# Kernel optimization log

Hardware: AMD Instinct MI355X
Metric: run time of the kernel (lower is better)

The kernel has to match this reference:

```python
import jax, jax.numpy as jnp
import numpy as np

V = 100000      # num nodes
E = 600000      # num edges (even: first half in-edges, second half out-edges)
D_IN = 128
D_OUT = 128
NREL2 = 100     # num_rel * 2
BN_EPS = 1e-5


def ccorr(a, b):
    # circular correlation along last dim: irfft(conj(rfft(a)) * rfft(b), n=d)
    d = a.shape[-1]
    return jnp.fft.irfft(jnp.conj(jnp.fft.rfft(a)) * jnp.fft.rfft(b), n=d).astype(a.dtype)


def setup_inputs() -> dict:
    key = jax.random.key(0)
    ks = jax.random.split(key, 12)
    return {
        "x": jax.random.normal(ks[0], (V, D_IN), dtype=jnp.float32),
        "rel_repr": jax.random.normal(ks[1], (NREL2, D_IN), dtype=jnp.float32),
        "edge_norm": jax.random.uniform(ks[2], (E,), dtype=jnp.float32),
        "in_w": jax.random.normal(ks[3], (D_IN, D_OUT), dtype=jnp.float32) * 0.05,
        "out_w": jax.random.normal(ks[4], (D_IN, D_OUT), dtype=jnp.float32) * 0.05,
        "loop_w": jax.random.normal(ks[5], (D_IN, D_OUT), dtype=jnp.float32) * 0.05,
        "w_rel": jax.random.normal(ks[6], (D_IN, D_OUT), dtype=jnp.float32) * 0.05,
        "loop_rel": jax.random.normal(ks[7], (1, D_IN), dtype=jnp.float32),
        "bias": jnp.zeros((D_OUT,), dtype=jnp.float32),
        "bn_gamma": jnp.ones((D_OUT,), dtype=jnp.float32),
        "bn_beta": jnp.zeros((D_OUT,), dtype=jnp.float32),
        "edge_src": jax.random.randint(ks[8], (E,), 0, V, dtype=jnp.int32),
        "edge_dst": jax.random.randint(ks[9], (E,), 0, V, dtype=jnp.int32),
        "edge_type": jax.random.randint(ks[10], (E,), 0, NREL2, dtype=jnp.int32),
    }


def reference(x, rel_repr, edge_norm, in_w, out_w, loop_w, w_rel, loop_rel,
              bias, bn_gamma, bn_beta, edge_src, edge_dst, edge_type):
    rel = rel_repr  # rel_wt is None (num_base=-1)
    # gather src features per edge and compose with relation embedding (corr)
    edge_data = ccorr(x[edge_src], rel[edge_type])             # [E, D_IN]
    half = edge_data.shape[0] // 2
    msg = jnp.concatenate(
        [edge_data[:half] @ in_w, edge_data[half:] @ out_w], axis=0
    ) * edge_norm[:, None]                                     # [E, D_OUT]
    # scatter-sum into destination nodes
    agg = jax.ops.segment_sum(msg, edge_dst, num_segments=V)   # [V, D_OUT]
    # self-loop term
    loop = ccorr(x, jnp.broadcast_to(loop_rel, x.shape)) @ loop_w
    h = (agg + loop) / 3.0 + bias
    # BatchNorm1d (training mode: batch stats, biased variance)
    mean = h.mean(axis=0)
    var = h.var(axis=0)
    h = (h - mean) * jax.lax.rsqrt(var + BN_EPS) * bn_gamma + bn_beta
    # act is identity; ltr=True -> project relations
    return h, rel @ w_rel
```

## Files before the change

kernel.cpp:

```cpp
#include <hip/hip_runtime.h>
#include <hip/hip_bf16.h>

#define D 128
constexpr int V_N    = 100000;
constexpr int E_N    = 600000;
constexpr int HALF_E = E_N / 2;
constexpr int NREL2  = 100;
constexpr int NBUCK  = 2 * NREL2;
constexpr float BN_EPS_F = 1e-5f;

constexpr int CHUNK  = 4096;
constexpr int NCHUNK = (E_N + CHUNK - 1) / CHUNK;

typedef short bf16x8  __attribute__((ext_vector_type(8)));
typedef float f32x16  __attribute__((ext_vector_type(16)));
typedef float f32x4v  __attribute__((ext_vector_type(4)));
typedef unsigned int uint32;

constexpr size_t MT_BYTES  = 201ull * D * D * 2;
constexpr size_t P_SS_OFF  = MT_BYTES;
constexpr size_t P_SD_OFF  = P_SS_OFF + (size_t)E_N * 4;
constexpr size_t P_SN_OFF  = P_SD_OFF + (size_t)E_N * 4;
constexpr size_t P_AGG_OFF = P_SN_OFF + (size_t)E_N * 4;
constexpr size_t AGG_BYTES = (size_t)V_N * D * 2;
constexpr size_t P_HIST_OFF = P_AGG_OFF;
constexpr size_t P_COFF_OFF = P_HIST_OFF + (size_t)NBUCK * NCHUNK * 4;
constexpr size_t P_CS_OFF  = P_AGG_OFF + AGG_BYTES;
constexpr size_t P_CQ_OFF  = P_CS_OFF + 512;
constexpr size_t P_CNT_OFF = P_CQ_OFF + 512;
constexpr size_t P_ST_OFF  = P_CNT_OFF + 1024;
constexpr size_t WS_NEED_PK = P_ST_OFF + 1024;

constexpr int LOOP_GRID2 = 782;
constexpr size_t P2_XBF  = (WS_NEED_PK + 255) & ~(size_t)255;
constexpr size_t P2_PSUM = P2_XBF + AGG_BYTES;
constexpr size_t P2_PSQ  = P2_PSUM + 128ull * LOOP_GRID2 * 4;
constexpr size_t WS_NEED2 = P2_PSQ + 128ull * LOOP_GRID2 * 4;

__device__ inline unsigned short f2bf(float f) {
    __hip_bfloat16 h = __float2bfloat16(f);
    return __builtin_bit_cast(unsigned short, h);
}
__device__ inline float bf2f(unsigned int u) {
    return __uint_as_float(u << 16);
}

__device__ inline int bucket_of(int e, const int* __restrict__ etype) {
    return etype[e] + (e < HALF_E ? 0 : NREL2);
}

__global__ __launch_bounds__(256) void k_hist_chunk(const int* __restrict__ etype,
                                                    int* __restrict__ hist) {
    __shared__ int h[NBUCK];
    for (int i = threadIdx.x; i < NBUCK; i += 256) h[i] = 0;
    __syncthreads();
    int c = blockIdx.x;
    int e0 = c * CHUNK;
#pragma unroll
    for (int r = 0; r < CHUNK / 256; r++) {
        int e = e0 + r * 256 + threadIdx.x;
        if (e < E_N) atomicAdd(&h[bucket_of(e, etype)], 1);
    }
    __syncthreads();
    for (int b = threadIdx.x; b < NBUCK; b += 256) hist[b * NCHUNK + c] = h[b];
}

__global__ void k_scan_bucket(const int* __restrict__ hist, int* __restrict__ chunkoff,
                              int* __restrict__ counts) {
    int b = blockIdx.x, lane = threadIdx.x;
    int acc = 0;
    for (int base = 0; base < NCHUNK; base += 64) {
        int c = base + lane;
        int v = (c < NCHUNK) ? hist[b * NCHUNK + c] : 0;
        int s = v;
#pragma unroll
        for (int off = 1; off < 64; off <<= 1) {
            int t = __shfl(s, lane - off, 64);
            if (lane >= off) s += t;
        }
        if (c < NCHUNK) chunkoff[b * NCHUNK + c] = acc + (s - v);
        acc += __shfl(s, 63, 64);
    }
    if (lane == 0) counts[b] = acc;
}

__global__ void k_scan(const int* __restrict__ counts, int* __restrict__ starts) {
    __shared__ int s[256];
    int i = threadIdx.x;
    int v = (i < NBUCK) ? counts[i] : 0;
    s[i] = v;
    __syncthreads();
    for (int off = 1; off < 256; off <<= 1) {
        int t = (i >= off) ? s[i - off] : 0;
        __syncthreads();
        s[i] += t;
        __syncthreads();
    }
    if (i < NBUCK) starts[i] = s[i] - v;
    if (i == 255) starts[NBUCK] = s[255];
}

__global__ __launch_bounds__(256) void k_scatter2(
    const int* __restrict__ src, const int* __restrict__ dst,
    const float* __restrict__ norm, const int* __restrict__ etype,
    const int* __restrict__ starts, const int* __restrict__ chunkoff,
    int* __restrict__ ssrc, int* __restrict__ sdst, float* __restrict__ snorm) {
    __shared__ int h[NBUCK];
    __shared__ int sbase[NBUCK];
    int c = blockIdx.x;
    for (int b = threadIdx.x; b < NBUCK; b += 256) {
        h[b] = 0;
        sbase[b] = starts[b] + chunkoff[b * NCHUNK + c];
    }
    __syncthreads();
    int e0 = c * CHUNK;
#pragma unroll
    for (int r = 0; r < CHUNK / 256; r++) {
        int e = e0 + r * 256 + threadIdx.x;
        if (e < E_N) {
            int b = bucket_of(e, etype);
            int rank = atomicAdd(&h[b], 1);
            int p = sbase[b] + rank;
            ssrc[p] = src[e]; sdst[p] = dst[e]; snorm[p] = norm[e];
        }
    }
}

__global__ __launch_bounds__(256) void k_xbf(const float* __restrict__ x,
                                             ushort* __restrict__ xbf) {
    const int N8 = V_N * D / 8;
    int i = blockIdx.x * 256 + threadIdx.x;
    if (i >= N8) return;
    f32x4v v0 = *(const f32x4v*)&x[(size_t)i * 8];
    f32x4v v1 = *(const f32x4v*)&x[(size_t)i * 8 + 4];
    union { ushort u[8]; uint4 q; } t;
    t.u[0] = f2bf(v0[0]); t.u[1] = f2bf(v0[1]); t.u[2] = f2bf(v0[2]); t.u[3] = f2bf(v0[3]);
    t.u[4] = f2bf(v1[0]); t.u[5] = f2bf(v1[1]); t.u[6] = f2bf(v1[2]); t.u[7] = f2bf(v1[3]);
    *(uint4*)&xbf[(size_t)i * 8] = t.q;
}

__global__ void k_build_M(const float* __restrict__ rel, const float* __restrict__ in_w,
                          const float* __restrict__ out_w, const float* __restrict__ loop_rel,
                          const float* __restrict__ loop_w, ushort* __restrict__ MT) {
    extern __shared__ float smem[];
    float* sW = smem;
    float* sR = smem + D * D;
    int b = blockIdx.x;
    const float* r = (b < NREL2) ? rel + (size_t)b * D
                   : (b < NBUCK) ? rel + (size_t)(b - NREL2) * D : loop_rel;
    const float* W = (b < NREL2) ? in_w : (b < NBUCK) ? out_w : loop_w;
    for (int i = threadIdx.x; i < D * D; i += blockDim.x) sW[i] = W[i];
    for (int i = threadIdx.x; i < D; i += blockDim.x) { float v = r[i]; sR[i] = v; sR[i + D] = v; }
    __syncthreads();
    int o  = threadIdx.x & 127;
    int jg = threadIdx.x >> 7;
    ushort* MTb = MT + (size_t)b * (D * D);
    for (int pass = 0; pass < 4; pass++) {
        int jbase = jg * 64 + pass * 16;
        float acc[16];
#pragma unroll
        for (int t = 0; t < 16; t++) acc[t] = 0.f;
        for (int k = 0; k < D; k++) {
            float w = sW[k * D + o];
#pragma unroll
            for (int t = 0; t < 16; t++) acc[t] += sR[jbase + t + k] * w;
        }
#pragma unroll
        for (int t = 0; t < 16; t++) MTb[(size_t)o * D + jbase + t] = f2bf(acc[t]);
    }
}

__global__ void k_relw(const float* __restrict__ rel, const float* __restrict__ w_rel,
                       float* __restrict__ out2) {
    int rr = blockIdx.x, o = threadIdx.x;
    float acc = 0.f;
    for (int k = 0; k < D; k++) acc += rel[rr * D + k] * w_rel[k * D + o];
    out2[rr * D + o] = acc;
}

constexpr int BPB = 8;

__global__ __launch_bounds__(256) void k_edge_pkb(
    const ushort* __restrict__ xbf, const ushort* __restrict__ MT,
    const int* __restrict__ starts, const int* __restrict__ ssrc,
    const int* __restrict__ sdst, const float* __restrict__ snorm,
    ushort* __restrict__ agg) {
    int wid  = threadIdx.x >> 6, lane = threadIdx.x & 63;
    int l31  = lane & 31, l5 = lane >> 5;
    int bucket = blockIdx.x / BPB;
    int sib    = (blockIdx.x % BPB) * 2 + (wid >> 1);
    int oh     = wid & 1;
    int bstart = starts[bucket], bend = starts[bucket + 1];
    const ushort* MTb = MT + (size_t)bucket * (D * D);
    int c0 = oh * 64 + 2 * l31;
    bf16x8 B0[8], B1[8];
#pragma unroll
    for (int kc = 0; kc < 8; kc++) {
        B0[kc] = *(const bf16x8*)&MTb[(size_t)c0 * D + kc * 16 + l5 * 8];
        B1[kc] = *(const bf16x8*)&MTb[(size_t)(c0 + 1) * D + kc * 16 + l5 * 8];
    }
    for (int tbase = bstart + sib * 32; tbase < bend; tbase += BPB * 2 * 32) {
        int nv = bend - tbase; if (nv > 32) nv = 32;
        int sr = ssrc[tbase + (l31 < nv ? l31 : 0)];
        const ushort* xr = xbf + (size_t)sr * D + l5 * 8;
        bf16x8 A[8];
#pragma unroll
        for (int kc = 0; kc < 8; kc++) A[kc] = *(const bf16x8*)(xr + kc * 16);
        f32x16 C0, C1;
#pragma unroll
        for (int i = 0; i < 16; i++) { C0[i] = 0.f; C1[i] = 0.f; }
#pragma unroll
        for (int kc = 0; kc < 8; kc++) {
            C0 = __builtin_amdgcn_mfma_f32_32x32x16_bf16(A[kc], B0[kc], C0, 0, 0, 0);
            C1 = __builtin_amdgcn_mfma_f32_32x32x16_bf16(A[kc], B1[kc], C1, 0, 0, 0);
        }
#pragma unroll
        for (int r = 0; r < 16; r++) {
            int rw = (r & 3) + 8 * (r >> 2) + 4 * l5;
            if (rw < nv) {
                float nm = snorm[tbase + rw];
                int   dv = sdst[tbase + rw];
                union { ushort u[2]; unsigned int w; } p;
                p.u[0] = f2bf(C0[r] * nm);
                p.u[1] = f2bf(C1[r] * nm);
                ushort* ap = agg + (size_t)dv * D + c0;
                asm volatile("global_atomic_pk_add_bf16 %0, %1, off"
                             :: "v"(ap), "v"(p.w) : "memory");
            }
        }
    }
}

__global__ __launch_bounds__(256) void k_loop_nb(
    const ushort* __restrict__ xbf, const ushort* __restrict__ MT,
    const float* __restrict__ bias, const ushort* __restrict__ agg,
    float* __restrict__ out, float* __restrict__ psum, float* __restrict__ psq) {
    __shared__ float lsum[128], lsq[128];
    if (threadIdx.x < 128) { lsum[threadIdx.x] = 0.f; lsq[threadIdx.x] = 0.f; }
    int wid = threadIdx.x >> 6, lane = threadIdx.x & 63;
    int l31 = lane & 31, l5 = lane >> 5;
    int oh  = wid & 1;
    int strm = blockIdx.x * 2 + (wid >> 1);
    const int NSTR = LOOP_GRID2 * 2;
    const ushort* MTb = MT + (size_t)NBUCK * (D * D);
    int ocol0 = oh * 64 + l31, ocol1 = oh * 64 + 32 + l31;
    bf16x8 B0[8], B1[8];
#pragma unroll
    for (int kc = 0; kc < 8; kc++) {
        B0[kc] = *(const bf16x8*)&MTb[(size_t)ocol0 * D + kc * 16 + l5 * 8];
        B1[kc] = *(const bf16x8*)&MTb[(size_t)ocol1 * D + kc * 16 + l5 * 8];
    }
    float b0 = bias[ocol0], b1 = bias[ocol1];
    float ps0 = 0.f, pq0 = 0.f, ps1 = 0.f, pq1 = 0.f;
    const int NT = V_N / 32;
    for (int tile = strm; tile < NT; tile += NSTR) {
        int tbase = tile * 32;
        const ushort* xr = xbf + (size_t)(tbase + l31) * D + l5 * 8;
        bf16x8 A[8];
#pragma unroll
        for (int kc = 0; kc < 8; kc++) A[kc] = *(const bf16x8*)(xr + kc * 16);
        f32x16 C0, C1;
#pragma unroll
        for (int i = 0; i < 16; i++) { C0[i] = 0.f; C1[i] = 0.f; }
#pragma unroll
        for (int kc = 0; kc < 8; kc++) {
            C0 = __builtin_amdgcn_mfma_f32_32x32x16_bf16(A[kc], B0[kc], C0, 0, 0, 0);
            C1 = __builtin_amdgcn_mfma_f32_32x32x16_bf16(A[kc], B1[kc], C1, 0, 0, 0);
        }
#pragma unroll
        for (int r = 0; r < 16; r++) {
            int rw = (r & 3) + 8 * (r >> 2) + 4 * l5;
            size_t i0 = (size_t)(tbase + rw) * D + ocol0;
            size_t i1 = (size_t)(tbase + rw) * D + ocol1;
            float h0 = (bf2f((uint32)agg[i0]) + C0[r]) * (1.f / 3.f) + b0;
            float h1 = (bf2f((uint32)agg[i1]) + C1[r]) * (1.f / 3.f) + b1;
            out[i0] = h0; out[i1] = h1;
            ps0 += h0; pq0 += h0 * h0;
            ps1 += h1; pq1 += h1 * h1;
        }
    }
    __syncthreads();
    atomicAdd(&lsum[ocol0], ps0); atomicAdd(&lsq[ocol0], pq0);
    atomicAdd(&lsum[ocol1], ps1); atomicAdd(&lsq[ocol1], pq1);
    __syncthreads();
    if (threadIdx.x < 128) {
        psum[(size_t)threadIdx.x * LOOP_GRID2 + blockIdx.x] = lsum[threadIdx.x];
        psq [(size_t)threadIdx.x * LOOP_GRID2 + blockIdx.x] = lsq [threadIdx.x];
    }
}

__global__ __launch_bounds__(256) void k_colreduce(
    const float* __restrict__ psum, const float* __restrict__ psq,
    float* __restrict__ colsum, float* __restrict__ colsq) {
    __shared__ float ls[256], lq[256];
    int c = blockIdx.x, tid = threadIdx.x;
    float s = 0.f, q = 0.f;
    for (int b = tid; b < LOOP_GRID2; b += 256) {
        s += psum[(size_t)c * LOOP_GRID2 + b];
        q += psq [(size_t)c * LOOP_GRID2 + b];
    }
    ls[tid] = s; lq[tid] = q;
    __syncthreads();
    for (int off = 128; off > 0; off >>= 1) {
        if (tid < off) { ls[tid] += ls[tid + off]; lq[tid] += lq[tid + off]; }
        __syncthreads();
    }
    if (tid == 0) { colsum[c] = ls[0]; colsq[c] = lq[0]; }
}

__global__ __launch_bounds__(256) void k_edge_pk(
    const float* __restrict__ x, const ushort* __restrict__ MT,
    const int* __restrict__ starts, const int* __restrict__ ssrc,
    const int* __restrict__ sdst, const float* __restrict__ snorm,
    ushort* __restrict__ agg) {
    int wid  = threadIdx.x >> 6, lane = threadIdx.x & 63;
    int l31  = lane & 31, l5 = lane >> 5;
    int bucket = blockIdx.x / BPB;
    int sib    = (blockIdx.x % BPB) * 2 + (wid >> 1);
    int oh     = wid & 1;
    int bstart = starts[bucket], bend = starts[bucket + 1];
    const ushort* MTb = MT + (size_t)bucket * (D * D);
    int c0 = oh * 64 + 2 * l31;
    bf16x8 B0[8], B1[8];
#pragma unroll
    for (int kc = 0; kc < 8; kc++) {
        B0[kc] = *(const bf16x8*)&MTb[(size_t)c0 * D + kc * 16 + l5 * 8];
        B1[kc] = *(const bf16x8*)&MTb[(size_t)(c0 + 1) * D + kc * 16 + l5 * 8];
    }
    for (int tbase = bstart + sib * 32; tbase < bend; tbase += BPB * 2 * 32) {
        int nv = bend - tbase; if (nv > 32) nv = 32;
        int sr = ssrc[tbase + (l31 < nv ? l31 : 0)];
        const float* xr = x + (size_t)sr * D + l5 * 8;
        bf16x8 A[8];
#pragma unroll
        for (int kc = 0; kc < 8; kc++) {
            f32x4v v0 = *(const f32x4v*)(xr + kc * 16);
            f32x4v v1 = *(const f32x4v*)(xr + kc * 16 + 4);
            union { bf16x8 v; ushort u[8]; } t;
            t.u[0] = f2bf(v0[0]); t.u[1] = f2bf(v0[1]); t.u[2] = f2bf(v0[2]); t.u[3] = f2bf(v0[3]);
            t.u[4] = f2bf(v1[0]); t.u[5] = f2bf(v1[1]); t.u[6] = f2bf(v1[2]); t.u[7] = f2bf(v1[3]);
            A[kc] = t.v;
        }
        f32x16 C0, C1;
#pragma unroll
        for (int i = 0; i < 16; i++) { C0[i] = 0.f; C1[i] = 0.f; }
#pragma unroll
        for (int kc = 0; kc < 8; kc++) {
            C0 = __builtin_amdgcn_mfma_f32_32x32x16_bf16(A[kc], B0[kc], C0, 0, 0, 0);
            C1 = __builtin_amdgcn_mfma_f32_32x32x16_bf16(A[kc], B1[kc], C1, 0, 0, 0);
        }
#pragma unroll
        for (int r = 0; r < 16; r++) {
            int rw = (r & 3) + 8 * (r >> 2) + 4 * l5;
            if (rw < nv) {
                float nm = snorm[tbase + rw];
                int   dv = sdst[tbase + rw];
                union { ushort u[2]; unsigned int w; } p;
                p.u[0] = f2bf(C0[r] * nm);
                p.u[1] = f2bf(C1[r] * nm);
                ushort* ap = agg + (size_t)dv * D + c0;
                asm volatile("global_atomic_pk_add_bf16 %0, %1, off"
                             :: "v"(ap), "v"(p.w) : "memory");
            }
        }
    }
}

constexpr int LOOP_GRID = 400;
__global__ __launch_bounds__(256) void k_loop_pk(
    const float* __restrict__ x, const ushort* __restrict__ MT,
    const float* __restrict__ bias, const ushort* __restrict__ agg,
    float* __restrict__ out, float* __restrict__ colsum, float* __restrict__ colsq) {
    int wid = threadIdx.x >> 6, lane = threadIdx.x & 63;
    int l31 = lane & 31, l5 = lane >> 5;
    int oh  = wid & 1;
    int strm = blockIdx.x * 2 + (wid >> 1);
    const int NSTR = LOOP_GRID * 2;
    const ushort* MTb = MT + (size_t)NBUCK * (D * D);
    int ocol0 = oh * 64 + l31, ocol1 = oh * 64 + 32 + l31;
    bf16x8 B0[8], B1[8];
#pragma unroll
    for (int kc = 0; kc < 8; kc++) {
        B0[kc] = *(const bf16x8*)&MTb[(size_t)ocol0 * D + kc * 16 + l5 * 8];
        B1[kc] = *(const bf16x8*)&MTb[(size_t)ocol1 * D + kc * 16 + l5 * 8];
    }
    float b0 = bias[ocol0], b1 = bias[ocol1];
    float ps0 = 0.f, pq0 = 0.f, ps1 = 0.f, pq1 = 0.f;
    const int NT = V_N / 32;
    for (int tile = strm; tile < NT; tile += NSTR) {
        int tbase = tile * 32;
        const float* xr = x + (size_t)(tbase + l31) * D + l5 * 8;
        bf16x8 A[8];
#pragma unroll
        for (int kc = 0; kc < 8; kc++) {
            f32x4v v0 = *(const f32x4v*)(xr + kc * 16);
            f32x4v v1 = *(const f32x4v*)(xr + kc * 16 + 4);
            union { bf16x8 v; ushort u[8]; } t;
            t.u[0] = f2bf(v0[0]); t.u[1] = f2bf(v0[1]); t.u[2] = f2bf(v0[2]); t.u[3] = f2bf(v0[3]);
            t.u[4] = f2bf(v1[0]); t.u[5] = f2bf(v1[1]); t.u[6] = f2bf(v1[2]); t.u[7] = f2bf(v1[3]);
            A[kc] = t.v;
        }
        f32x16 C0, C1;
#pragma unroll
        for (int i = 0; i < 16; i++) { C0[i] = 0.f; C1[i] = 0.f; }
#pragma unroll
        for (int kc = 0; kc < 8; kc++) {
            C0 = __builtin_amdgcn_mfma_f32_32x32x16_bf16(A[kc], B0[kc], C0, 0, 0, 0);
            C1 = __builtin_amdgcn_mfma_f32_32x32x16_bf16(A[kc], B1[kc], C1, 0, 0, 0);
        }
#pragma unroll
        for (int r = 0; r < 16; r++) {
            int rw = (r & 3) + 8 * (r >> 2) + 4 * l5;
            size_t i0 = (size_t)(tbase + rw) * D + ocol0;
            size_t i1 = (size_t)(tbase + rw) * D + ocol1;
            float h0 = (bf2f((uint32)agg[i0]) + C0[r]) * (1.f / 3.f) + b0;
            float h1 = (bf2f((uint32)agg[i1]) + C1[r]) * (1.f / 3.f) + b1;
            out[i0] = h0; out[i1] = h1;
            ps0 += h0; pq0 += h0 * h0;
            ps1 += h1; pq1 += h1 * h1;
        }
    }
    atomicAdd(&colsum[ocol0], ps0); atomicAdd(&colsq[ocol0], pq0);
    atomicAdd(&colsum[ocol1], ps1); atomicAdd(&colsq[ocol1], pq1);
}

__global__ void k_bn(float* __restrict__ out, const float* __restrict__ colsum,
                     const float* __restrict__ colsq, const float* __restrict__ gamma,
                     const float* __restrict__ beta) {
    const size_t N4 = (size_t)V_N * D / 4;
    size_t stride = (size_t)gridDim.x * blockDim.x;
    for (size_t q = (size_t)blockIdx.x * blockDim.x + threadIdx.x; q < N4; q += stride) {
        int c4 = (int)(q & 31);
        float4 s  = *(const float4*)&colsum[c4 * 4];
        float4 sq = *(const float4*)&colsq[c4 * 4];
        float4 g  = *(const float4*)&gamma[c4 * 4];
        float4 be = *(const float4*)&beta[c4 * 4];
        float4 h  = *(float4*)&out[q * 4];
        const float inv = 1.f / (float)V_N;
        float m0 = s.x * inv, m1 = s.y * inv, m2 = s.z * inv, m3 = s.w * inv;
        float r0 = rsqrtf(sq.x * inv - m0 * m0 + BN_EPS_F);
        float r1 = rsqrtf(sq.y * inv - m1 * m1 + BN_EPS_F);
        float r2 = rsqrtf(sq.z * inv - m2 * m2 + BN_EPS_F);
        float r3 = rsqrtf(sq.w * inv - m3 * m3 + BN_EPS_F);
        h.x = (h.x - m0) * r0 * g.x + be.x;
        h.y = (h.y - m1) * r1 * g.y + be.y;
        h.z = (h.z - m2) * r2 * g.z + be.z;
        h.w = (h.w - m3) * r3 * g.w + be.w;
        *(float4*)&out[q * 4] = h;
    }
}

extern "C" void kernel_launch(void* const* d_in, const int* in_sizes, int n_in,
                              void* d_out, int out_size, void* d_ws, size_t ws_size,
                              hipStream_t stream) {
    const float* x        = (const float*)d_in[0];
    const float* rel      = (const float*)d_in[1];
    const float* enorm    = (const float*)d_in[2];
    const float* in_w     = (const float*)d_in[3];
    const float* out_w    = (const float*)d_in[4];
    const float* loop_w   = (const float*)d_in[5];
    const float* w_rel    = (const float*)d_in[6];
    const float* loop_rel = (const float*)d_in[7];
    const float* bias     = (const float*)d_in[8];
    const float* gamma    = (const float*)d_in[9];
    const float* beta     = (const float*)d_in[10];
    const int*   esrc     = (const int*)d_in[11];
    const int*   edst     = (const int*)d_in[12];
    const int*   etype    = (const int*)d_in[13];
    float* out = (float*)d_out;
    char*  ws  = (char*)d_ws;

    const int gM = 201, smem = (D * D + 256) * sizeof(float);

    ushort* MT     = (ushort*)(ws + 0);
    int*    ssrc   = (int*)(ws + P_SS_OFF);
    int*    sdst   = (int*)(ws + P_SD_OFF);
    float*  snorm  = (float*)(ws + P_SN_OFF);
    ushort* aggbf  = (ushort*)(ws + P_AGG_OFF);
    int*    hist   = (int*)(ws + P_HIST_OFF);
    int*    coff   = (int*)(ws + P_COFF_OFF);
    float*  colsum = (float*)(ws + P_CS_OFF);
    float*  colsq  = (float*)(ws + P_CQ_OFF);
    int*    counts = (int*)(ws + P_CNT_OFF);
    int*    starts = (int*)(ws + P_ST_OFF);

    k_hist_chunk<<<NCHUNK, 256, 0, stream>>>(etype, hist);
    k_scan_bucket<<<NBUCK, 64, 0, stream>>>(hist, coff, counts);
    k_scan<<<1, 256, 0, stream>>>(counts, starts);
    k_scatter2<<<NCHUNK, 256, 0, stream>>>(esrc, edst, enorm, etype, starts, coff,
                                           ssrc, sdst, snorm);
    hipMemsetAsync(ws + P_AGG_OFF, 0, AGG_BYTES, stream);

    k_build_M<<<gM, 256, smem, stream>>>(rel, in_w, out_w, loop_rel, loop_w, MT);
    k_relw<<<NREL2, D, 0, stream>>>(rel, w_rel, out + (size_t)V_N * D);

    if (ws_size >= WS_NEED2) {
        ushort* xbf  = (ushort*)(ws + P2_XBF);
        float*  psum = (float*)(ws + P2_PSUM);
        float*  psq  = (float*)(ws + P2_PSQ);

        k_xbf<<<(V_N * D / 8 + 255) / 256, 256, 0, stream>>>(x, xbf);
        k_edge_pkb<<<NBUCK * BPB, 256, 0, stream>>>(xbf, MT, starts, ssrc, sdst, snorm, aggbf);
        k_loop_nb<<<LOOP_GRID2, 256, 0, stream>>>(xbf, MT, bias, aggbf, out, psum, psq);
        k_colreduce<<<128, 256, 0, stream>>>(psum, psq, colsum, colsq);
        k_bn<<<2048, 256, 0, stream>>>(out, colsum, colsq, gamma, beta);
    } else {
        hipMemsetAsync(ws + P_CS_OFF, 0, 1024, stream);
        k_edge_pk<<<NBUCK * BPB, 256, 0, stream>>>(x, MT, starts, ssrc, sdst, snorm, aggbf);
        k_loop_pk<<<LOOP_GRID, 256, 0, stream>>>(x, MT, bias, aggbf, out, colsum, colsq);
        k_bn<<<2048, 256, 0, stream>>>(out, colsum, colsq, gamma, beta);
    }
}
```

Baseline: 458.6 us.

## Replace bf16 atomic scatter with CSR segmented sum over stored messages

Adds a path, used when the workspace is large enough, that builds a CSR (degree count, scan, permutation) over destination nodes. The edge GEMM then writes per-edge bf16 messages to a buffer, and a per-node kernel sums them in fp32 with no atomics. It also merges the M-matrix build, the relation projection and the x-to-bf16 conversion into one setup launch. The loop kernel now uses a paired-column layout so agg reads and out writes are vectorised. The cost is a 150MB message buffer written then read back, several extra CSR-build kernels, and random gathers in the segmented sum. The path is skipped if the workspace is too small.

Measured after the change: 507.2 us. 10.6% more time.

```diff
diff --git a/kernel.cpp b/kernel.cpp
--- a/kernel.cpp
+++ b/kernel.cpp
@@ -17,12 +17,14 @@
 typedef float f32x4v  __attribute__((ext_vector_type(4)));
 typedef unsigned int uint32;
 
+constexpr int LOOP_GRID2 = 782;
 constexpr size_t MT_BYTES  = 201ull * D * D * 2;
+constexpr size_t AGG_BYTES = (size_t)V_N * D * 2;
+
 constexpr size_t P_SS_OFF  = MT_BYTES;
 constexpr size_t P_SD_OFF  = P_SS_OFF + (size_t)E_N * 4;
 constexpr size_t P_SN_OFF  = P_SD_OFF + (size_t)E_N * 4;
 constexpr size_t P_AGG_OFF = P_SN_OFF + (size_t)E_N * 4;
-constexpr size_t AGG_BYTES = (size_t)V_N * D * 2;
 constexpr size_t P_HIST_OFF = P_AGG_OFF;
 constexpr size_t P_COFF_OFF = P_HIST_OFF + (size_t)NBUCK * NCHUNK * 4;
 constexpr size_t P_CS_OFF  = P_AGG_OFF + AGG_BYTES;
@@ -30,13 +32,35 @@
 constexpr size_t P_CNT_OFF = P_CQ_OFF + 512;
 constexpr size_t P_ST_OFF  = P_CNT_OFF + 1024;
 constexpr size_t WS_NEED_PK = P_ST_OFF + 1024;
-
-constexpr int LOOP_GRID2 = 782;
 constexpr size_t P2_XBF  = (WS_NEED_PK + 255) & ~(size_t)255;
 constexpr size_t P2_PSUM = P2_XBF + AGG_BYTES;
 constexpr size_t P2_PSQ  = P2_PSUM + 128ull * LOOP_GRID2 * 4;
 constexpr size_t WS_NEED2 = P2_PSQ + 128ull * LOOP_GRID2 * 4;
 
+constexpr size_t V4_SS   = MT_BYTES;
+constexpr size_t V4_SD   = V4_SS + (size_t)E_N * 4;
+constexpr size_t V4_SN   = V4_SD + (size_t)E_N * 4;
+constexpr size_t V4_XBF  = V4_SN + (size_t)E_N * 4;
+constexpr size_t V4_AGG  = V4_XBF + AGG_BYTES;
+constexpr size_t V4_DEG  = V4_AGG + AGG_BYTES;
+constexpr size_t V4_CS   = V4_DEG + (size_t)V_N * 4;
+constexpr size_t V4_CQ   = V4_CS + 512;
+constexpr size_t V4_RP   = V4_CQ + 512;
+constexpr size_t V4_CUR  = V4_RP + (size_t)(V_N + 16) * 4;
+constexpr size_t V4_EIDX = V4_CUR + (size_t)V_N * 4;
+constexpr size_t V4_HIST = V4_EIDX + (size_t)E_N * 4;
+constexpr size_t V4_COFF = V4_HIST + (size_t)NBUCK * NCHUNK * 4;
+constexpr size_t V4_CNT  = V4_COFF + (size_t)NBUCK * NCHUNK * 4;
+constexpr size_t V4_ST   = V4_CNT + 1024;
+constexpr size_t V4_BSUM = V4_ST + 1024;
+constexpr size_t V4_PSUM = (V4_BSUM + 1024 + 255) & ~(size_t)255;
+constexpr size_t V4_PSQ  = V4_PSUM + 128ull * LOOP_GRID2 * 4;
+constexpr size_t V4_MSG  = (V4_PSQ + 128ull * LOOP_GRID2 * 4 + 255) & ~(size_t)255;
+constexpr size_t WS_NEED4 = V4_MSG + (size_t)E_N * D * 2;
+
+constexpr int SCAN_ELEMS = 1024;
+constexpr int NSCANB = (V_N + SCAN_ELEMS - 1) / SCAN_ELEMS;
+
 __device__ inline unsigned short f2bf(float f) {
     __hip_bfloat16 h = __float2bfloat16(f);
     return __builtin_bit_cast(unsigned short, h);
@@ -44,7 +68,6 @@
 __device__ inline float bf2f(unsigned int u) {
     return __uint_as_float(u << 16);
 }
-
 __device__ inline int bucket_of(int e, const int* __restrict__ etype) {
     return etype[e] + (e < HALF_E ? 0 : NREL2);
 }
@@ -126,59 +149,267 @@
     }
 }
 
-__global__ __launch_bounds__(256) void k_xbf(const float* __restrict__ x,
-                                             ushort* __restrict__ xbf) {
-    const int N8 = V_N * D / 8;
+constexpr int SETUP_XBF_BLOCKS = 800;
+constexpr int SETUP_GRID = 201 + 50 + SETUP_XBF_BLOCKS;
+__global__ void k_setup(const float* __restrict__ x, const float* __restrict__ rel,
+                        const float* __restrict__ in_w, const float* __restrict__ out_w,
+                        const float* __restrict__ loop_rel, const float* __restrict__ loop_w,
+                        const float* __restrict__ w_rel, ushort* __restrict__ MT,
+                        ushort* __restrict__ xbf, float* __restrict__ out2) {
+    extern __shared__ float smem[];
+    int blk = blockIdx.x;
+    if (blk < 201) {
+        float* sW = smem;
+        float* sR = smem + D * D;
+        int b = blk;
+        const float* r = (b < NREL2) ? rel + (size_t)b * D
+                       : (b < NBUCK) ? rel + (size_t)(b - NREL2) * D : loop_rel;
+        const float* W = (b < NREL2) ? in_w : (b < NBUCK) ? out_w : loop_w;
+        for (int i = threadIdx.x; i < D * D; i += blockDim.x) sW[i] = W[i];
+        for (int i = threadIdx.x; i < D; i += blockDim.x) { float v = r[i]; sR[i] = v; sR[i + D] = v; }
+        __syncthreads();
+        int o  = threadIdx.x & 127;
+        int jg = threadIdx.x >> 7;
+        ushort* MTb = MT + (size_t)b * (D * D);
+        for (int pass = 0; pass < 4; pass++) {
+            int jbase = jg * 64 + pass * 16;
+            float acc[16];
+#pragma unroll
+            for (int t = 0; t < 16; t++) acc[t] = 0.f;
+            for (int k = 0; k < D; k++) {
+                float w = sW[k * D + o];
+#pragma unroll
+                for (int t = 0; t < 16; t++) acc[t] += sR[jbase + t + k] * w;
+            }
+#pragma unroll
+            for (int t = 0; t < 16; t++) MTb[(size_t)o * D + jbase + t] = f2bf(acc[t]);
+        }
+    } else if (blk < 251) {
+        int rr = (blk - 201) * 2 + (threadIdx.x >> 7);
+        int o  = threadIdx.x & 127;
+        float acc = 0.f;
+        for (int k = 0; k < D; k++) acc += rel[rr * D + k] * w_rel[k * D + o];
+        out2[rr * D + o] = acc;
+    } else {
+        const int N8 = V_N * D / 8;
+        for (int i = (blk - 251) * 256 + threadIdx.x; i < N8; i += SETUP_XBF_BLOCKS * 256) {
+            f32x4v v0 = *(const f32x4v*)&x[(size_t)i * 8];
+            f32x4v v1 = *(const f32x4v*)&x[(size_t)i * 8 + 4];
+            union { ushort u[8]; uint4 q; } t;
+            t.u[0] = f2bf(v0[0]); t.u[1] = f2bf(v0[1]); t.u[2] = f2bf(v0[2]); t.u[3] = f2bf(v0[3]);
+            t.u[4] = f2bf(v1[0]); t.u[5] = f2bf(v1[1]); t.u[6] = f2bf(v1[2]); t.u[7] = f2bf(v1[3]);
+            *(uint4*)&xbf[(size_t)i * 8] = t.q;
+        }
+    }
+}
+
+__global__ __launch_bounds__(256) void k_deg(const int* __restrict__ sdst,
+                                             int* __restrict__ deg) {
+    int p = blockIdx.x * 256 + threadIdx.x;
+    if (p < E_N) atomicAdd(&deg[sdst[p]], 1);
+}
+
+__global__ __launch_bounds__(256) void k_scan1(const int* __restrict__ deg,
+                                               int* __restrict__ rowptr,
+                                               int* __restrict__ blocksum) {
+    __shared__ int s[256];
+    int blk = blockIdx.x, tid = threadIdx.x;
+    int base = blk * SCAN_ELEMS + tid * 4;
+    int v[4]; int tot = 0;
+#pragma unroll
+    for (int j = 0; j < 4; j++) { int i = base + j; v[j] = (i < V_N) ? deg[i] : 0; tot += v[j]; }
+    s[tid] = tot;
+    __syncthreads();
+    for (int off = 1; off < 256; off <<= 1) {
+        int t = (tid >= off) ? s[tid - off] : 0;
+        __syncthreads();
+        s[tid] += t;
+        __syncthreads();
+    }
+    int run = s[tid] - tot;
+#pragma unroll
+    for (int j = 0; j < 4; j++) { int i = base + j; if (i < V_N) rowptr[i] = run; run += v[j]; }
+    if (tid == 255) blocksum[blk] = s[255];
+}
+
+__global__ void k_scan2(int* __restrict__ blocksum) {
+    __shared__ int s[128];
+    int i = threadIdx.x;
+    int v = (i < NSCANB) ? blocksum[i] : 0;
+    s[i] = v;
+    __syncthreads();
+    for (int off = 1; off < 128; off <<= 1) {
+        int t = (i >= off) ? s[i - off] : 0;
+        __syncthreads();
+        s[i] += t;
+        __syncthreads();
+    }
+    if (i < NSCANB) blocksum[i] = s[i] - v;
+}
+
+__global__ __launch_bounds__(256) void k_scan3(int* __restrict__ rowptr,
+                                               const int* __restrict__ blocksum,
+                                               int* __restrict__ cursor) {
     int i = blockIdx.x * 256 + threadIdx.x;
-    if (i >= N8) return;
-    f32x4v v0 = *(const f32x4v*)&x[(size_t)i * 8];
-    f32x4v v1 = *(const f32x4v*)&x[(size_t)i * 8 + 4];
-    union { ushort u[8]; uint4 q; } t;
-    t.u[0] = f2bf(v0[0]); t.u[1] = f2bf(v0[1]); t.u[2] = f2bf(v0[2]); t.u[3] = f2bf(v0[3]);
-    t.u[4] = f2bf(v1[0]); t.u[5] = f2bf(v1[1]); t.u[6] = f2bf(v1[2]); t.u[7] = f2bf(v1[3]);
-    *(uint4*)&xbf[(size_t)i * 8] = t.q;
-}
-
-__global__ void k_build_M(const float* __restrict__ rel, const float* __restrict__ in_w,
-                          const float* __restrict__ out_w, const float* __restrict__ loop_rel,
-                          const float* __restrict__ loop_w, ushort* __restrict__ MT) {
-    extern __shared__ float smem[];
-    float* sW = smem;
-    float* sR = smem + D * D;
-    int b = blockIdx.x;
-    const float* r = (b < NREL2) ? rel + (size_t)b * D
-                   : (b < NBUCK) ? rel + (size_t)(b - NREL2) * D : loop_rel;
-    const float* W = (b < NREL2) ? in_w : (b < NBUCK) ? out_w : loop_w;
-    for (int i = threadIdx.x; i < D * D; i += blockDim.x) sW[i] = W[i];
-    for (int i = threadIdx.x; i < D; i += blockDim.x) { float v = r[i]; sR[i] = v; sR[i + D] = v; }
-    __syncthreads();
-    int o  = threadIdx.x & 127;
-    int jg = threadIdx.x >> 7;
-    ushort* MTb = MT + (size_t)b * (D * D);
-    for (int pass = 0; pass < 4; pass++) {
-        int jbase = jg * 64 + pass * 16;
-        float acc[16];
-#pragma unroll
-        for (int t = 0; t < 16; t++) acc[t] = 0.f;
-        for (int k = 0; k < D; k++) {
-            float w = sW[k * D + o];
-#pragma unroll
-            for (int t = 0; t < 16; t++) acc[t] += sR[jbase + t + k] * w;
-        }
-#pragma unroll
-        for (int t = 0; t < 16; t++) MTb[(size_t)o * D + jbase + t] = f2bf(acc[t]);
-    }
-}
-
-__global__ void k_relw(const float* __restrict__ rel, const float* __restrict__ w_rel,
-                       float* __restrict__ out2) {
-    int rr = blockIdx.x, o = threadIdx.x;
-    float acc = 0.f;
-    for (int k = 0; k < D; k++) acc += rel[rr * D + k] * w_rel[k * D + o];
-    out2[rr * D + o] = acc;
+    if (i < V_N) {
+        int r = rowptr[i] + blocksum[i >> 10];
+        rowptr[i] = r; cursor[i] = r;
+    }
+    if (i == 0) rowptr[V_N] = E_N;
+}
+
+__global__ __launch_bounds__(256) void k_perm(const int* __restrict__ sdst,
+                                              int* __restrict__ cursor,
+                                              int* __restrict__ eidx) {
+    int p = blockIdx.x * 256 + threadIdx.x;
+    if (p < E_N) {
+        int slot = atomicAdd(&cursor[sdst[p]], 1);
+        eidx[slot] = p;
+    }
 }
 
 constexpr int BPB = 8;
+
+__global__ __launch_bounds__(256) void k_edge_st(
+    const ushort* __restrict__ xbf, const ushort* __restrict__ MT,
+    const int* __restrict__ starts, const int* __restrict__ ssrc,
+    const float* __restrict__ snorm, uint32* __restrict__ msg32) {
+    int wid  = threadIdx.x >> 6, lane = threadIdx.x & 63;
+    int l31  = lane & 31, l5 = lane >> 5;
+    int bucket = blockIdx.x / BPB;
+    int sib    = (blockIdx.x % BPB) * 2 + (wid >> 1);
+    int oh     = wid & 1;
+    int bstart = starts[bucket], bend = starts[bucket + 1];
+    const ushort* MTb = MT + (size_t)bucket * (D * D);
+    int c0 = oh * 64 + 2 * l31;
+    bf16x8 B0[8], B1[8];
+#pragma unroll
+    for (int kc = 0; kc < 8; kc++) {
+        B0[kc] = *(const bf16x8*)&MTb[(size_t)c0 * D + kc * 16 + l5 * 8];
+        B1[kc] = *(const bf16x8*)&MTb[(size_t)(c0 + 1) * D + kc * 16 + l5 * 8];
+    }
+    for (int tbase = bstart + sib * 32; tbase < bend; tbase += BPB * 2 * 32) {
+        int nv = bend - tbase; if (nv > 32) nv = 32;
+        int sr = ssrc[tbase + (l31 < nv ? l31 : 0)];
+        const ushort* xr = xbf + (size_t)sr * D + l5 * 8;
+        bf16x8 A[8];
+#pragma unroll
+        for (int kc = 0; kc < 8; kc++) A[kc] = *(const bf16x8*)(xr + kc * 16);
+        f32x16 C0, C1;
+#pragma unroll
+        for (int i = 0; i < 16; i++) { C0[i] = 0.f; C1[i] = 0.f; }
+#pragma unroll
+        for (int kc = 0; kc < 8; kc++) {
+            C0 = __builtin_amdgcn_mfma_f32_32x32x16_bf16(A[kc], B0[kc], C0, 0, 0, 0);
+            C1 = __builtin_amdgcn_mfma_f32_32x32x16_bf16(A[kc], B1[kc], C1, 0, 0, 0);
+        }
+#pragma unroll
+        for (int r = 0; r < 16; r++) {
+            int rw = (r & 3) + 8 * (r >> 2) + 4 * l5;
+            if (rw < nv) {
+                int p = tbase + rw;
+                float nm = snorm[p];
+                uint32 u = (uint32)f2bf(C0[r] * nm) | ((uint32)f2bf(C1[r] * nm) << 16);
+                msg32[(size_t)p * 64 + oh * 32 + l31] = u;
+            }
+        }
+    }
+}
+
+__global__ __launch_bounds__(256) void k_segsum(
+    const uint32* __restrict__ msg32, const int* __restrict__ eidx,
+    const int* __restrict__ rowptr, uint32* __restrict__ agg32) {
+    int v = blockIdx.x * 4 + (threadIdx.x >> 6);
+    if (v >= V_N) return;
+    int lane = threadIdx.x & 63;
+    int s = rowptr[v], e = rowptr[v + 1];
+    float a0 = 0.f, a1 = 0.f;
+    for (int i = s; i < e; i++) {
+        int p = eidx[i];
+        uint32 u = msg32[(size_t)p * 64 + lane];
+        a0 += bf2f(u & 0xffffu); a1 += bf2f(u >> 16);
+    }
+    agg32[(size_t)v * 64 + lane] = (uint32)f2bf(a0) | ((uint32)f2bf(a1) << 16);
+}
+
+__global__ __launch_bounds__(256) void k_loop_pair(
+    const ushort* __restrict__ xbf, const ushort* __restrict__ MT,
+    const float* __restrict__ bias, const uint32* __restrict__ agg32,
+    float* __restrict__ out, float* __restrict__ psum, float* __restrict__ psq) {
+    __shared__ float lsum[128], lsq[128];
+    if (threadIdx.x < 128) { lsum[threadIdx.x] = 0.f; lsq[threadIdx.x] = 0.f; }
+    int wid = threadIdx.x >> 6, lane = threadIdx.x & 63;
+    int l31 = lane & 31, l5 = lane >> 5;
+    int oh  = wid & 1;
+    int strm = blockIdx.x * 2 + (wid >> 1);
+    const int NSTR = LOOP_GRID2 * 2;
+    const ushort* MTb = MT + (size_t)NBUCK * (D * D);
+    int c0 = oh * 64 + 2 * l31;
+    int jj = oh * 32 + l31;
+    bf16x8 B0[8], B1[8];
+#pragma unroll
+    for (int kc = 0; kc < 8; kc++) {
+        B0[kc] = *(const bf16x8*)&MTb[(size_t)c0 * D + kc * 16 + l5 * 8];
+        B1[kc] = *(const bf16x8*)&MTb[(size_t)(c0 + 1) * D + kc * 16 + l5 * 8];
+    }
+    float b0 = bias[c0], b1 = bias[c0 + 1];
+    float ps0 = 0.f, pq0 = 0.f, ps1 = 0.f, pq1 = 0.f;
+    const int NT = V_N / 32;
+    for (int tile = strm; tile < NT; tile += NSTR) {
+        int tbase = tile * 32;
+        const ushort* xr = xbf + (size_t)(tbase + l31) * D + l5 * 8;
+        bf16x8 A[8];
+#pragma unroll
+        for (int kc = 0; kc < 8; kc++) A[kc] = *(const bf16x8*)(xr + kc * 16);
+        f32x16 C0, C1;
+#pragma unroll
+        for (int i = 0; i < 16; i++) { C0[i] = 0.f; C1[i] = 0.f; }
+#pragma unroll
+        for (int kc = 0; kc < 8; kc++) {
+            C0 = __builtin_amdgcn_mfma_f32_32x32x16_bf16(A[kc], B0[kc], C0, 0, 0, 0);
+            C1 = __builtin_amdgcn_mfma_f32_32x32x16_bf16(A[kc], B1[kc], C1, 0, 0, 0);
+        }
+#pragma unroll
+        for (int r = 0; r < 16; r++) {
+            int rw = (r & 3) + 8 * (r >> 2) + 4 * l5;
+            int row = tbase + rw;
+            uint32 u = agg32[(size_t)row * 64 + jj];
+            float h0 = (bf2f(u & 0xffffu) + C0[r]) * (1.f / 3.f) + b0;
+            float h1 = (bf2f(u >> 16)     + C1[r]) * (1.f / 3.f) + b1;
+            float2 hv = make_float2(h0, h1);
+            *(float2*)&out[(size_t)row * D + c0] = hv;
+            ps0 += h0; pq0 += h0 * h0;
+            ps1 += h1; pq1 += h1 * h1;
+        }
+    }
+    __syncthreads();
+    atomicAdd(&lsum[c0], ps0); atomicAdd(&lsq[c0], pq0);
+    atomicAdd(&lsum[c0 + 1], ps1); atomicAdd(&lsq[c0 + 1], pq1);
+    __syncthreads();
+    if (threadIdx.x < 128) {
+        psum[(size_t)threadIdx.x * LOOP_GRID2 + blockIdx.x] = lsum[threadIdx.x];
+        psq [(size_t)threadIdx.x * LOOP_GRID2 + blockIdx.x] = lsq [threadIdx.x];
+    }
+}
+
+__global__ __launch_bounds__(256) void k_colreduce(
+    const float* __restrict__ psum, const float* __restrict__ psq,
+    float* __restrict__ colsum, float* __restrict__ colsq) {
+    __shared__ float ls[256], lq[256];
+    int c = blockIdx.x, tid = threadIdx.x;
+    float s = 0.f, q = 0.f;
+    for (int b = tid; b < LOOP_GRID2; b += 256) {
+        s += psum[(size_t)c * LOOP_GRID2 + b];
+        q += psq [(size_t)c * LOOP_GRID2 + b];
+    }
+    ls[tid] = s; lq[tid] = q;
+    __syncthreads();
+    for (int off = 128; off > 0; off >>= 1) {
+        if (tid < off) { ls[tid] += ls[tid + off]; lq[tid] += lq[tid + off]; }
+        __syncthreads();
+    }
+    if (tid == 0) { colsum[c] = ls[0]; colsq[c] = lq[0]; }
+}
 
 __global__ __launch_bounds__(256) void k_edge_pkb(
     const ushort* __restrict__ xbf, const ushort* __restrict__ MT,
@@ -229,199 +460,6 @@
             }
         }
     }
-}
-
-__global__ __launch_bounds__(256) void k_loop_nb(
-    const ushort* __restrict__ xbf, const ushort* __restrict__ MT,
-    const float* __restrict__ bias, const ushort* __restrict__ agg,
-    float* __restrict__ out, float* __restrict__ psum, float* __restrict__ psq) {
-    __shared__ float lsum[128], lsq[128];
-    if (threadIdx.x < 128) { lsum[threadIdx.x] = 0.f; lsq[threadIdx.x] = 0.f; }
-    int wid = threadIdx.x >> 6, lane = threadIdx.x & 63;
-    int l31 = lane & 31, l5 = lane >> 5;
-    int oh  = wid & 1;
-    int strm = blockIdx.x * 2 + (wid >> 1);
-    const int NSTR = LOOP_GRID2 * 2;
-    const ushort* MTb = MT + (size_t)NBUCK * (D * D);
-    int ocol0 = oh * 64 + l31, ocol1 = oh * 64 + 32 + l31;
-    bf16x8 B0[8], B1[8];
-#pragma unroll
-    for (int kc = 0; kc < 8; kc++) {
-        B0[kc] = *(const bf16x8*)&MTb[(size_t)ocol0 * D + kc * 16 + l5 * 8];
-        B1[kc] = *(const bf16x8*)&MTb[(size_t)ocol1 * D + kc * 16 + l5 * 8];
-    }
-    float b0 = bias[ocol0], b1 = bias[ocol1];
-    float ps0 = 0.f, pq0 = 0.f, ps1 = 0.f, pq1 = 0.f;
-    const int NT = V_N / 32;
-    for (int tile = strm; tile < NT; tile += NSTR) {
-        int tbase = tile * 32;
-        const ushort* xr = xbf + (size_t)(tbase + l31) * D + l5 * 8;
-        bf16x8 A[8];
-#pragma unroll
-        for (int kc = 0; kc < 8; kc++) A[kc] = *(const bf16x8*)(xr + kc * 16);
-        f32x16 C0, C1;
-#pragma unroll
-        for (int i = 0; i < 16; i++) { C0[i] = 0.f; C1[i] = 0.f; }
-#pragma unroll
-        for (int kc = 0; kc < 8; kc++) {
-            C0 = __builtin_amdgcn_mfma_f32_32x32x16_bf16(A[kc], B0[kc], C0, 0, 0, 0);
-            C1 = __builtin_amdgcn_mfma_f32_32x32x16_bf16(A[kc], B1[kc], C1, 0, 0, 0);
-        }
-#pragma unroll
-        for (int r = 0; r < 16; r++) {
-            int rw = (r & 3) + 8 * (r >> 2) + 4 * l5;
-            size_t i0 = (size_t)(tbase + rw) * D + ocol0;
-            size_t i1 = (size_t)(tbase + rw) * D + ocol1;
-            float h0 = (bf2f((uint32)agg[i0]) + C0[r]) * (1.f / 3.f) + b0;
-            float h1 = (bf2f((uint32)agg[i1]) + C1[r]) * (1.f / 3.f) + b1;
-            out[i0] = h0; out[i1] = h1;
-            ps0 += h0; pq0 += h0 * h0;
-            ps1 += h1; pq1 += h1 * h1;
-        }
-    }
-    __syncthreads();
-    atomicAdd(&lsum[ocol0], ps0); atomicAdd(&lsq[ocol0], pq0);
-    atomicAdd(&lsum[ocol1], ps1); atomicAdd(&lsq[ocol1], pq1);
-    __syncthreads();
-    if (threadIdx.x < 128) {
-        psum[(size_t)threadIdx.x * LOOP_GRID2 + blockIdx.x] = lsum[threadIdx.x];
-        psq [(size_t)threadIdx.x * LOOP_GRID2 + blockIdx.x] = lsq [threadIdx.x];
-    }
-}
-
-__global__ __launch_bounds__(256) void k_colreduce(
-    const float* __restrict__ psum, const float* __restrict__ psq,
-    float* __restrict__ colsum, float* __restrict__ colsq) {
-    __shared__ float ls[256], lq[256];
-    int c = blockIdx.x, tid = threadIdx.x;
-    float s = 0.f, q = 0.f;
-    for (int b = tid; b < LOOP_GRID2; b += 256) {
-        s += psum[(size_t)c * LOOP_GRID2 + b];
-        q += psq [(size_t)c * LOOP_GRID2 + b];
-    }
-    ls[tid] = s; lq[tid] = q;
-    __syncthreads();
-    for (int off = 128; off > 0; off >>= 1) {
-        if (tid < off) { ls[tid] += ls[tid + off]; lq[tid] += lq[tid + off]; }
-        __syncthreads();
-    }
-    if (tid == 0) { colsum[c] = ls[0]; colsq[c] = lq[0]; }
-}
-
-__global__ __launch_bounds__(256) void k_edge_pk(
-    const float* __restrict__ x, const ushort* __restrict__ MT,
-    const int* __restrict__ starts, const int* __restrict__ ssrc,
-    const int* __restrict__ sdst, const float* __restrict__ snorm,
-    ushort* __restrict__ agg) {
-    int wid  = threadIdx.x >> 6, lane = threadIdx.x & 63;
-    int l31  = lane & 31, l5 = lane >> 5;
-    int bucket = blockIdx.x / BPB;
-    int sib    = (blockIdx.x % BPB) * 2 + (wid >> 1);
-    int oh     = wid & 1;
-    int bstart = starts[bucket], bend = starts[bucket + 1];
-    const ushort* MTb = MT + (size_t)bucket * (D * D);
-    int c0 = oh * 64 + 2 * l31;
-    bf16x8 B0[8], B1[8];
-#pragma unroll
-    for (int kc = 0; kc < 8; kc++) {
-        B0[kc] = *(const bf16x8*)&MTb[(size_t)c0 * D + kc * 16 + l5 * 8];
-        B1[kc] = *(const bf16x8*)&MTb[(size_t)(c0 + 1) * D + kc * 16 + l5 * 8];
-    }
-    for (int tbase = bstart + sib * 32; tbase < bend; tbase += BPB * 2 * 32) {
-        int nv = bend - tbase; if (nv > 32) nv = 32;
-        int sr = ssrc[tbase + (l31 < nv ? l31 : 0)];
-        const float* xr = x + (size_t)sr * D + l5 * 8;
-        bf16x8 A[8];
-#pragma unroll
-        for (int kc = 0; kc < 8; kc++) {
-            f32x4v v0 = *(const f32x4v*)(xr + kc * 16);
-            f32x4v v1 = *(const f32x4v*)(xr + kc * 16 + 4);
-            union { bf16x8 v; ushort u[8]; } t;
-            t.u[0] = f2bf(v0[0]); t.u[1] = f2bf(v0[1]); t.u[2] = f2bf(v0[2]); t.u[3] = f2bf(v0[3]);
-            t.u[4] = f2bf(v1[0]); t.u[5] = f2bf(v1[1]); t.u[6] = f2bf(v1[2]); t.u[7] = f2bf(v1[3]);
-            A[kc] = t.v;
-        }
-        f32x16 C0, C1;
-#pragma unroll
-        for (int i = 0; i < 16; i++) { C0[i] = 0.f; C1[i] = 0.f; }
-#pragma unroll
-        for (int kc = 0; kc < 8; kc++) {
-            C0 = __builtin_amdgcn_mfma_f32_32x32x16_bf16(A[kc], B0[kc], C0, 0, 0, 0);
-            C1 = __builtin_amdgcn_mfma_f32_32x32x16_bf16(A[kc], B1[kc], C1, 0, 0, 0);
-        }
-#pragma unroll
-        for (int r = 0; r < 16; r++) {
-            int rw = (r & 3) + 8 * (r >> 2) + 4 * l5;
-            if (rw < nv) {
-                float nm = snorm[tbase + rw];
-                int   dv = sdst[tbase + rw];
-                union { ushort u[2]; unsigned int w; } p;
-                p.u[0] = f2bf(C0[r] * nm);
-                p.u[1] = f2bf(C1[r] * nm);
-                ushort* ap = agg + (size_t)dv * D + c0;
-                asm volatile("global_atomic_pk_add_bf16 %0, %1, off"
-                             :: "v"(ap), "v"(p.w) : "memory");
-            }
-        }
-    }
-}
-
-constexpr int LOOP_GRID = 400;
-__global__ __launch_bounds__(256) void k_loop_pk(
-    const float* __restrict__ x, const ushort* __restrict__ MT,
-    const float* __restrict__ bias, const ushort* __restrict__ agg,
-    float* __restrict__ out, float* __restrict__ colsum, float* __restrict__ colsq) {
-    int wid = threadIdx.x >> 6, lane = threadIdx.x & 63;
-    int l31 = lane & 31, l5 = lane >> 5;
-    int oh  = wid & 1;
-    int strm = blockIdx.x * 2 + (wid >> 1);
-    const int NSTR = LOOP_GRID * 2;
-    const ushort* MTb = MT + (size_t)NBUCK * (D * D);
-    int ocol0 = oh * 64 + l31, ocol1 = oh * 64 + 32 + l31;
-    bf16x8 B0[8], B1[8];
-#pragma unroll
-    for (int kc = 0; kc < 8; kc++) {
-        B0[kc] = *(const bf16x8*)&MTb[(size_t)ocol0 * D + kc * 16 + l5 * 8];
-        B1[kc] = *(const bf16x8*)&MTb[(size_t)ocol1 * D + kc * 16 + l5 * 8];
-    }
-    float b0 = bias[ocol0], b1 = bias[ocol1];
-    float ps0 = 0.f, pq0 = 0.f, ps1 = 0.f, pq1 = 0.f;
-    const int NT = V_N / 32;
-    for (int tile = strm; tile < NT; tile += NSTR) {
-        int tbase = tile * 32;
-        const float* xr = x + (size_t)(tbase + l31) * D + l5 * 8;
-        bf16x8 A[8];
-#pragma unroll
-        for (int kc = 0; kc < 8; kc++) {
-            f32x4v v0 = *(const f32x4v*)(xr + kc * 16);
-            f32x4v v1 = *(const f32x4v*)(xr + kc * 16 + 4);
-            union { bf16x8 v; ushort u[8]; } t;
-            t.u[0] = f2bf(v0[0]); t.u[1] = f2bf(v0[1]); t.u[2] = f2bf(v0[2]); t.u[3] = f2bf(v0[3]);
-            t.u[4] = f2bf(v1[0]); t.u[5] = f2bf(v1[1]); t.u[6] = f2bf(v1[2]); t.u[7] = f2bf(v1[3]);
-            A[kc] = t.v;
-        }
-        f32x16 C0, C1;
-#pragma unroll
-        for (int i = 0; i < 16; i++) { C0[i] = 0.f; C1[i] = 0.f; }
-#pragma unroll
-        for (int kc = 0; kc < 8; kc++) {
-            C0 = __builtin_amdgcn_mfma_f32_32x32x16_bf16(A[kc], B0[kc], C0, 0, 0, 0);
-            C1 = __builtin_amdgcn_mfma_f32_32x32x16_bf16(A[kc], B1[kc], C1, 0, 0, 0);
-        }
-#pragma unroll
-        for (int r = 0; r < 16; r++) {
-            int rw = (r & 3) + 8 * (r >> 2) + 4 * l5;
-            size_t i0 = (size_t)(tbase + rw) * D + ocol0;
-            size_t i1 = (size_t)(tbase + rw) * D + ocol1;
-            float h0 = (bf2f((uint32)agg[i0]) + C0[r]) * (1.f / 3.f) + b0;
-            float h1 = (bf2f((uint32)agg[i1]) + C1[r]) * (1.f / 3.f) + b1;
-            out[i0] = h0; out[i1] = h1;
-            ps0 += h0; pq0 += h0 * h0;
-            ps1 += h1; pq1 += h1 * h1;
-        }
-    }
-    atomicAdd(&colsum[ocol0], ps0); atomicAdd(&colsq[ocol0], pq0);
-    atomicAdd(&colsum[ocol1], ps1); atomicAdd(&colsq[ocol1], pq1);
 }
 
 __global__ void k_bn(float* __restrict__ out, const float* __restrict__ colsum,
@@ -470,44 +508,80 @@
     float* out = (float*)d_out;
     char*  ws  = (char*)d_ws;
 
-    const int gM = 201, smem = (D * D + 256) * sizeof(float);
-
-    ushort* MT     = (ushort*)(ws + 0);
-    int*    ssrc   = (int*)(ws + P_SS_OFF);
-    int*    sdst   = (int*)(ws + P_SD_OFF);
-    float*  snorm  = (float*)(ws + P_SN_OFF);
-    ushort* aggbf  = (ushort*)(ws + P_AGG_OFF);
-    int*    hist   = (int*)(ws + P_HIST_OFF);
-    int*    coff   = (int*)(ws + P_COFF_OFF);
-    float*  colsum = (float*)(ws + P_CS_OFF);
-    float*  colsq  = (float*)(ws + P_CQ_OFF);
-    int*    counts = (int*)(ws + P_CNT_OFF);
-    int*    starts = (int*)(ws + P_ST_OFF);
-
-    k_hist_chunk<<<NCHUNK, 256, 0, stream>>>(etype, hist);
-    k_scan_bucket<<<NBUCK, 64, 0, stream>>>(hist, coff, counts);
-    k_scan<<<1, 256, 0, stream>>>(counts, starts);
-    k_scatter2<<<NCHUNK, 256, 0, stream>>>(esrc, edst, enorm, etype, starts, coff,
-                                           ssrc, sdst, snorm);
-    hipMemsetAsync(ws + P_AGG_OFF, 0, AGG_BYTES, stream);
-
-    k_build_M<<<gM, 256, smem, stream>>>(rel, in_w, out_w, loop_rel, loop_w, MT);
-    k_relw<<<NREL2, D, 0, stream>>>(rel, w_rel, out + (size_t)V_N * D);
-
-    if (ws_size >= WS_NEED2) {
-        ushort* xbf  = (ushort*)(ws + P2_XBF);
-        float*  psum = (float*)(ws + P2_PSUM);
-        float*  psq  = (float*)(ws + P2_PSQ);
-
-        k_xbf<<<(V_N * D / 8 + 255) / 256, 256, 0, stream>>>(x, xbf);
-        k_edge_pkb<<<NBUCK * BPB, 256, 0, stream>>>(xbf, MT, starts, ssrc, sdst, snorm, aggbf);
-        k_loop_nb<<<LOOP_GRID2, 256, 0, stream>>>(xbf, MT, bias, aggbf, out, psum, psq);
+    const int smem = (D * D + 256) * sizeof(float);
+    const int gE = (E_N + 255) / 256;
+
+    if (ws_size >= WS_NEED4) {
+        ushort* MT     = (ushort*)(ws + 0);
+        int*    ssrc   = (int*)(ws + V4_SS);
+        int*    sdst   = (int*)(ws + V4_SD);
+        float*  snorm  = (float*)(ws + V4_SN);
+        ushort* xbf    = (ushort*)(ws + V4_XBF);
+        uint32* agg32  = (uint32*)(ws + V4_AGG);
+        int*    deg    = (int*)(ws + V4_DEG);
+        float*  colsum = (float*)(ws + V4_CS);
+        float*  colsq  = (float*)(ws + V4_CQ);
+        int*    rowptr = (int*)(ws + V4_RP);
+        int*    cursor = (int*)(ws + V4_CUR);
+        int*    eidx   = (int*)(ws + V4_EIDX);
+        int*    hist   = (int*)(ws + V4_HIST);
+        int*    coff   = (int*)(ws + V4_COFF);
+        int*    counts = (int*)(ws + V4_CNT);
+        int*    starts = (int*)(ws + V4_ST);
+        int*    bsum   = (int*)(ws + V4_BSUM);
+        float*  psum   = (float*)(ws + V4_PSUM);
+        float*  psq    = (float*)(ws + V4_PSQ);
+        uint32* msg32  = (uint32*)(ws + V4_MSG);
+
+        hipMemsetAsync(ws + V4_DEG, 0, (size_t)V_N * 4, stream);
+
+        k_hist_chunk<<<NCHUNK, 256, 0, stream>>>(etype, hist);
+        k_scan_bucket<<<NBUCK, 64, 0, stream>>>(hist, coff, counts);
+        k_scan<<<1, 256, 0, stream>>>(counts, starts);
+        k_scatter2<<<NCHUNK, 256, 0, stream>>>(esrc, edst, enorm, etype, starts, coff,
+                                               ssrc, sdst, snorm);
+        k_setup<<<SETUP_GRID, 256, smem, stream>>>(x, rel, in_w, out_w, loop_rel, loop_w,
+                                                   w_rel, MT, xbf, out + (size_t)V_N * D);
+        k_deg<<<gE, 256, 0, stream>>>(sdst, deg);
+        k_scan1<<<NSCANB, 256, 0, stream>>>(deg, rowptr, bsum);
+        k_scan2<<<1, 128, 0, stream>>>(bsum);
+        k_scan3<<<(V_N + 255) / 256, 256, 0, stream>>>(rowptr, bsum, cursor);
+        k_perm<<<gE, 256, 0, stream>>>(sdst, cursor, eidx);
+
+        k_edge_st<<<NBUCK * BPB, 256, 0, stream>>>(xbf, MT, starts, ssrc, snorm, msg32);
+        k_segsum<<<(V_N + 3) / 4, 256, 0, stream>>>(msg32, eidx, rowptr, agg32);
+
+        k_loop_pair<<<LOOP_GRID2, 256, 0, stream>>>(xbf, MT, bias, agg32, out, psum, psq);
         k_colreduce<<<128, 256, 0, stream>>>(psum, psq, colsum, colsq);
         k_bn<<<2048, 256, 0, stream>>>(out, colsum, colsq, gamma, beta);
     } else {
-        hipMemsetAsync(ws + P_CS_OFF, 0, 1024, stream);
-        k_edge_pk<<<NBUCK * BPB, 256, 0, stream>>>(x, MT, starts, ssrc, sdst, snorm, aggbf);
-        k_loop_pk<<<LOOP_GRID, 256, 0, stream>>>(x, MT, bias, aggbf, out, colsum, colsq);
+        ushort* MT     = (ushort*)(ws + 0);
+        int*    ssrc   = (int*)(ws + P_SS_OFF);
+        int*    sdst   = (int*)(ws + P_SD_OFF);
+        float*  snorm  = (float*)(ws + P_SN_OFF);
+        ushort* aggbf  = (ushort*)(ws + P_AGG_OFF);
+        uint32* agg32  = (uint32*)(ws + P_AGG_OFF);
+        int*    hist   = (int*)(ws + P_HIST_OFF);
+        int*    coff   = (int*)(ws + P_COFF_OFF);
+        float*  colsum = (float*)(ws + P_CS_OFF);
+        float*  colsq  = (float*)(ws + P_CQ_OFF);
+        int*    counts = (int*)(ws + P_CNT_OFF);
+        int*    starts = (int*)(ws + P_ST_OFF);
+        ushort* xbf    = (ushort*)(ws + P2_XBF);
+        float*  psum   = (float*)(ws + P2_PSUM);
+        float*  psq    = (float*)(ws + P2_PSQ);
+
+        k_hist_chunk<<<NCHUNK, 256, 0, stream>>>(etype, hist);
+        k_scan_bucket<<<NBUCK, 64, 0, stream>>>(hist, coff, counts);
+        k_scan<<<1, 256, 0, stream>>>(counts, starts);
+        k_scatter2<<<NCHUNK, 256, 0, stream>>>(esrc, edst, enorm, etype, starts, coff,
+                                               ssrc, sdst, snorm);
+        hipMemsetAsync(ws + P_AGG_OFF, 0, AGG_BYTES, stream);
+        k_setup<<<SETUP_GRID, 256, smem, stream>>>(x, rel, in_w, out_w, loop_rel, loop_w,
+                                                   w_rel, MT, xbf, out + (size_t)V_N * D);
+        k_edge_pkb<<<NBUCK * BPB, 256, 0, stream>>>(xbf, MT, starts, ssrc, sdst, snorm, aggbf);
+        k_loop_pair<<<LOOP_GRID2, 256, 0, stream>>>(xbf, MT, bias, agg32, out, psum, psq);
+        k_colreduce<<<128, 256, 0, stream>>>(psum, psq, colsum, colsq);
         k_bn<<<2048, 256, 0, stream>>>(out, colsum, colsq, gamma, beta);
     }
 }
```
